# Kernel optimization log

Hardware: AMD Instinct MI355X
Metric: run time of the kernel (lower is better)

Reference implementation:

```python
import jax, jax.numpy as jnp
from jax import lax
import numpy as np

STATE_DIM, LATENT_DIM, HIDDEN_DIM = 18, 3, 16
BN_EPS = 1e-5


def _xavier(key, out_dim, in_dim):
    a = (6.0 / (in_dim + out_dim)) ** 0.5
    return jax.random.uniform(key, (out_dim, in_dim), minval=-a, maxval=a, dtype=jnp.float32)


def setup_inputs() -> dict:
    key = jax.random.key(0)
    ks = jax.random.split(key, 12)
    B, S, T = 4096, 256, 64
    inp = {
        "x_sequence": jax.random.normal(ks[0], (B, S, STATE_DIM), dtype=jnp.float32),
        "t_span": jnp.linspace(0.0, 6.3, T, dtype=jnp.float32),
        # encoder: Linear(18->16), ReLU, (Dropout off), BatchNorm1d(16, eval), Linear(16->3)
        "enc_w1": _xavier(ks[1], HIDDEN_DIM, STATE_DIM), "enc_b1": jnp.zeros((HIDDEN_DIM,), jnp.float32),
        "enc_bn_g": jnp.ones((HIDDEN_DIM,), jnp.float32), "enc_bn_b": jnp.zeros((HIDDEN_DIM,), jnp.float32),
        "enc_bn_m": jnp.zeros((HIDDEN_DIM,), jnp.float32), "enc_bn_v": jnp.ones((HIDDEN_DIM,), jnp.float32),
        "enc_w2": _xavier(ks[2], LATENT_DIM, HIDDEN_DIM), "enc_b2": jnp.zeros((LATENT_DIM,), jnp.float32),
        # decoder: Linear(3->16), ReLU, BN(16, eval), Linear(16->18)
        "dec_w1": _xavier(ks[3], HIDDEN_DIM, LATENT_DIM), "dec_b1": jnp.zeros((HIDDEN_DIM,), jnp.float32),
        "dec_bn_g": jnp.ones((HIDDEN_DIM,), jnp.float32), "dec_bn_b": jnp.zeros((HIDDEN_DIM,), jnp.float32),
        "dec_bn_m": jnp.zeros((HIDDEN_DIM,), jnp.float32), "dec_bn_v": jnp.ones((HIDDEN_DIM,), jnp.float32),
        "dec_w2": _xavier(ks[4], STATE_DIM, HIDDEN_DIM), "dec_b2": jnp.zeros((STATE_DIM,), jnp.float32),
        # ode_func: Linear(3->8), Tanh, Linear(8->3)
        "ode_w1": _xavier(ks[5], HIDDEN_DIM // 2, LATENT_DIM), "ode_b1": jnp.zeros((HIDDEN_DIM // 2,), jnp.float32),
        "ode_w2": _xavier(ks[6], LATENT_DIM, HIDDEN_DIM // 2), "ode_b2": jnp.zeros((LATENT_DIM,), jnp.float32),
        # perturbation classifier: Linear(3->4), ReLU, Linear(4->1), Sigmoid
        "cls_w1": _xavier(ks[7], 4, LATENT_DIM), "cls_b1": jnp.zeros((4,), jnp.float32),
        "cls_w2": _xavier(ks[8], 1, 4), "cls_b2": jnp.zeros((1,), jnp.float32),
    }
    return inp


def _bn_eval(x, g, b, m, v):
    return (x - m) * (g / jnp.sqrt(v + BN_EPS)) + b


def reference(x_sequence, t_span,
              enc_w1, enc_b1, enc_bn_g, enc_bn_b, enc_bn_m, enc_bn_v, enc_w2, enc_b2,
              dec_w1, dec_b1, dec_bn_g, dec_bn_b, dec_bn_m, dec_bn_v, dec_w2, dec_b2,
              ode_w1, ode_b1, ode_w2, ode_b2,
              cls_w1, cls_b1, cls_w2, cls_b2):
    B, S, D = x_sequence.shape
    T = t_span.shape[0]

    def encode(x):  # [N, 18] -> [N, 3]
        h = jax.nn.relu(x @ enc_w1.T + enc_b1)
        h = _bn_eval(h, enc_bn_g, enc_bn_b, enc_bn_m, enc_bn_v)
        return h @ enc_w2.T + enc_b2

    def decode(z):  # [N, 3] -> [N, 18]
        h = jax.nn.relu(z @ dec_w1.T + dec_b1)
        h = _bn_eval(h, dec_bn_g, dec_bn_b, dec_bn_m, dec_bn_v)
        return h @ dec_w2.T + dec_b2

    def ode_func(z):  # [B, 3] -> [B, 3]
        return jnp.tanh(z @ ode_w1.T + ode_b1) @ ode_w2.T + ode_b2

    x_flat = x_sequence.reshape(-1, D)              # [B*S, 18]
    z_flat = encode(x_flat)                         # [B*S, 3]
    z_seq = z_flat.reshape(B, S, LATENT_DIM)
    z0 = z_seq[:, -1, :]                            # [B, 3]

    # explicit Euler integration: z <- z + 0.1 * f(z), T steps
    def step(z, _):
        z_next = z + 0.1 * ode_func(z)
        return z_next, z_next

    _, z_traj = lax.scan(step, z0, None, length=T)  # [T, B, 3]
    z_pred = jnp.transpose(z_traj, (1, 0, 2))       # [B, T, 3]

    x_recon = decode(z_flat).reshape(B, S, D)
    x_pred = decode(z_pred.reshape(-1, LATENT_DIM)).reshape(B, T, D)

    z_mean = jnp.mean(z_seq, axis=1)                # [B, 3]
    h = jax.nn.relu(z_mean @ cls_w1.T + cls_b1)
    perturbation_prob = jax.nn.sigmoid(h @ cls_w2.T + cls_b2)  # [B, 1]

    return (x_recon, x_pred, perturbation_prob, z_seq)
```

## Files before the change

kernel.cpp:

```cpp
#include <hip/hip_runtime.h>
#include <math.h>

constexpr int Bn = 4096, Sn = 256, Tn = 64;
constexpr int Dn = 18, Hn = 16, Ln = 3;
constexpr float EPS = 1e-5f;

constexpr size_t OFF_XP   = (size_t)Bn * Sn * Dn;
constexpr size_t OFF_PROB = OFF_XP + (size_t)Bn * Tn * Dn;
constexpr size_t OFF_ZS   = OFF_PROB + (size_t)Bn;

__device__ __forceinline__ float fast_tanh(float x) {
    float ax = fabsf(x);
    float e  = __expf(-2.0f * ax);
    float r  = (1.0f - e) / (1.0f + e);
    return copysignf(r, x);
}

__global__ __launch_bounds__(256) void k1_encdec(
    const float* __restrict__ x,
    const float* __restrict__ ew1, const float* __restrict__ eb1,
    const float* __restrict__ eg,  const float* __restrict__ ebb,
    const float* __restrict__ em,  const float* __restrict__ ev,
    const float* __restrict__ ew2, const float* __restrict__ eb2,
    const float* __restrict__ dw1, const float* __restrict__ db1,
    const float* __restrict__ dg,  const float* __restrict__ dbn,
    const float* __restrict__ dm,  const float* __restrict__ dv,
    const float* __restrict__ dw2, const float* __restrict__ db2,
    const float* __restrict__ cw1, const float* __restrict__ cb1,
    const float* __restrict__ cw2, const float* __restrict__ cb2,
    float* __restrict__ xrec, float* __restrict__ prob, float* __restrict__ zseq)
{
    const int b = blockIdx.x;
    const int s = threadIdx.x;
    constexpr int TILE_F  = Sn * Dn;
    constexpr int TILE_F4 = TILE_F / 4;

    __shared__ float xt[TILE_F];
    __shared__ float esc[Hn], esh[Hn], dsc[Hn], dsh[Hn];
    __shared__ float red[4][3];

    if (s < Hn) {
        float sc = eg[s] / sqrtf(ev[s] + EPS);
        esc[s] = sc; esh[s] = ebb[s] - em[s] * sc;
        float sd = dg[s] / sqrtf(dv[s] + EPS);
        dsc[s] = sd; dsh[s] = dbn[s] - dm[s] * sd;
    }

    const float4* xg  = reinterpret_cast<const float4*>(x + (size_t)b * TILE_F);
    float4*       xt4 = reinterpret_cast<float4*>(xt);
    #pragma unroll
    for (int i = s; i < TILE_F4; i += 256) xt4[i] = xg[i];
    __syncthreads();

    float xv[Dn];
    #pragma unroll
    for (int k = 0; k < Dn; ++k) xv[k] = xt[s * Dn + k];

    float h[Hn];
    #pragma unroll
    for (int j = 0; j < Hn; ++j) {
        float a = eb1[j];
        #pragma unroll
        for (int k = 0; k < Dn; ++k) a = fmaf(ew1[j*Dn + k], xv[k], a);
        a = fmaxf(a, 0.0f);
        h[j] = fmaf(a, esc[j], esh[j]);
    }
    float z0 = eb2[0], z1 = eb2[1], z2 = eb2[2];
    #pragma unroll
    for (int j = 0; j < Hn; ++j) {
        z0 = fmaf(ew2[0*Hn + j], h[j], z0);
        z1 = fmaf(ew2[1*Hn + j], h[j], z1);
        z2 = fmaf(ew2[2*Hn + j], h[j], z2);
    }
    float* zp = zseq + ((size_t)b * Sn + s) * Ln;
    zp[0] = z0; zp[1] = z1; zp[2] = z2;

    float h2[Hn];
    #pragma unroll
    for (int j = 0; j < Hn; ++j) {
        float a = fmaf(dw1[j*Ln + 0], z0, db1[j]);
        a = fmaf(dw1[j*Ln + 1], z1, a);
        a = fmaf(dw1[j*Ln + 2], z2, a);
        a = fmaxf(a, 0.0f);
        h2[j] = fmaf(a, dsc[j], dsh[j]);
    }
    #pragma unroll
    for (int m = 0; m < Dn; ++m) {
        float a = db2[m];
        #pragma unroll
        for (int j = 0; j < Hn; ++j) a = fmaf(dw2[m*Hn + j], h2[j], a);
        xt[s * Dn + m] = a;
    }
    __syncthreads();

    float4* og = reinterpret_cast<float4*>(xrec + (size_t)b * TILE_F);
    #pragma unroll
    for (int i = s; i < TILE_F4; i += 256) og[i] = xt4[i];

    float r0 = z0, r1 = z1, r2 = z2;
    #pragma unroll
    for (int off = 32; off > 0; off >>= 1) {
        r0 += __shfl_down(r0, off);
        r1 += __shfl_down(r1, off);
        r2 += __shfl_down(r2, off);
    }
    const int lane = s & 63, wid = s >> 6;
    if (lane == 0) { red[wid][0] = r0; red[wid][1] = r1; red[wid][2] = r2; }
    __syncthreads();
    if (s == 0) {
        float m0 = (red[0][0] + red[1][0] + red[2][0] + red[3][0]) * (1.0f / Sn);
        float m1 = (red[0][1] + red[1][1] + red[2][1] + red[3][1]) * (1.0f / Sn);
        float m2 = (red[0][2] + red[1][2] + red[2][2] + red[3][2]) * (1.0f / Sn);
        float logit = cb2[0];
        #pragma unroll
        for (int j = 0; j < 4; ++j) {
            float a = fmaf(cw1[j*3 + 0], m0, cb1[j]);
            a = fmaf(cw1[j*3 + 1], m1, a);
            a = fmaf(cw1[j*3 + 2], m2, a);
            a = fmaxf(a, 0.0f);
            logit = fmaf(cw2[j], a, logit);
        }
        prob[b] = 1.0f / (1.0f + __expf(-logit));
    }
}

__global__ __launch_bounds__(256) void k2_ode(
    const float* __restrict__ zseq,
    const float* __restrict__ ow1, const float* __restrict__ ob1,
    const float* __restrict__ ow2, const float* __restrict__ ob2,
    float* __restrict__ zscr, int zlayout)
{
    const int b = blockIdx.x * blockDim.x + threadIdx.x;
    const float* zp = zseq + ((size_t)b * Sn + (Sn - 1)) * Ln;
    float z0 = zp[0], z1 = zp[1], z2 = zp[2];

    float w1[8][3], bb1[8], w2v[3][8], bb2[3];
    #pragma unroll
    for (int j = 0; j < 8; ++j) {
        bb1[j] = ob1[j];
        #pragma unroll
        for (int k = 0; k < 3; ++k) w1[j][k] = ow1[j*3 + k];
    }
    #pragma unroll
    for (int i = 0; i < 3; ++i) {
        bb2[i] = ob2[i];
        #pragma unroll
        for (int j = 0; j < 8; ++j) w2v[i][j] = ow2[i*8 + j];
    }

    for (int t = 0; t < Tn; ++t) {
        float a[8];
        #pragma unroll
        for (int j = 0; j < 8; ++j) {
            float u = fmaf(w1[j][0], z0, bb1[j]);
            u = fmaf(w1[j][1], z1, u);
            u = fmaf(w1[j][2], z2, u);
            a[j] = fast_tanh(u);
        }
        float d0 = bb2[0], d1 = bb2[1], d2 = bb2[2];
        #pragma unroll
        for (int j = 0; j < 8; ++j) {
            d0 = fmaf(w2v[0][j], a[j], d0);
            d1 = fmaf(w2v[1][j], a[j], d1);
            d2 = fmaf(w2v[2][j], a[j], d2);
        }
        z0 = fmaf(0.1f, d0, z0);
        z1 = fmaf(0.1f, d1, z1);
        z2 = fmaf(0.1f, d2, z2);
        size_t idx = (zlayout == 0) ? ((size_t)t * Bn + b) * Ln
                                    : ((size_t)b * Tn + t) * Dn;
        zscr[idx + 0] = z0; zscr[idx + 1] = z1; zscr[idx + 2] = z2;
    }
}

__global__ __launch_bounds__(256) void k3_decpred(
    const float* __restrict__ dw1, const float* __restrict__ db1,
    const float* __restrict__ dg,  const float* __restrict__ dbn,
    const float* __restrict__ dm,  const float* __restrict__ dv,
    const float* __restrict__ dw2, const float* __restrict__ db2,
    const float* __restrict__ zscr, int zlayout,
    float* __restrict__ xpred)
{
    const int r = blockIdx.x * blockDim.x + threadIdx.x;
    const int s = threadIdx.x;
    constexpr int TILE_F  = 256 * Dn;
    constexpr int TILE_F4 = TILE_F / 4;

    __shared__ float ot[TILE_F];
    __shared__ float dsc[Hn], dsh[Hn];
    if (s < Hn) {
        float sd = dg[s] / sqrtf(dv[s] + EPS);
        dsc[s] = sd;
        dsh[s] = dbn[s] - dm[s] * sd;
    }
    __syncthreads();

    const int bb = r / Tn, tt = r % Tn;
    size_t zidx = (zlayout == 0) ? ((size_t)tt * Bn + bb) * Ln
                                 : (size_t)r * Dn;
    float z0 = zscr[zidx + 0], z1 = zscr[zidx + 1], z2 = zscr[zidx + 2];

    float h2[Hn];
    #pragma unroll
    for (int j = 0; j < Hn; ++j) {
        float a = fmaf(dw1[j*Ln + 0], z0, db1[j]);
        a = fmaf(dw1[j*Ln + 1], z1, a);
        a = fmaf(dw1[j*Ln + 2], z2, a);
        a = fmaxf(a, 0.0f);
        h2[j] = fmaf(a, dsc[j], dsh[j]);
    }
    #pragma unroll
    for (int m = 0; m < Dn; ++m) {
        float a = db2[m];
        #pragma unroll
        for (int j = 0; j < Hn; ++j) a = fmaf(dw2[m*Hn + j], h2[j], a);
        ot[s * Dn + m] = a;
    }
    __syncthreads();

    float4* og = reinterpret_cast<float4*>(xpred + (size_t)blockIdx.x * TILE_F);
    const float4* ot4 = reinterpret_cast<const float4*>(ot);
    #pragma unroll
    for (int i = s; i < TILE_F4; i += 256) og[i] = ot4[i];
}

extern "C" void kernel_launch(void* const* d_in, const int* in_sizes, int n_in,
                              void* d_out, int out_size, void* d_ws, size_t ws_size,
                              hipStream_t stream)
{
    const float* x   = (const float*)d_in[0];
    const float* ew1 = (const float*)d_in[2];
    const float* eb1 = (const float*)d_in[3];
    const float* eg  = (const float*)d_in[4];
    const float* ebb = (const float*)d_in[5];
    const float* em  = (const float*)d_in[6];
    const float* ev  = (const float*)d_in[7];
    const float* ew2 = (const float*)d_in[8];
    const float* eb2 = (const float*)d_in[9];
    const float* dw1 = (const float*)d_in[10];
    const float* db1 = (const float*)d_in[11];
    const float* dg  = (const float*)d_in[12];
    const float* dbn = (const float*)d_in[13];
    const float* dm  = (const float*)d_in[14];
    const float* dv  = (const float*)d_in[15];
    const float* dw2 = (const float*)d_in[16];
    const float* db2 = (const float*)d_in[17];
    const float* ow1 = (const float*)d_in[18];
    const float* ob1 = (const float*)d_in[19];
    const float* ow2 = (const float*)d_in[20];
    const float* ob2 = (const float*)d_in[21];
    const float* cw1 = (const float*)d_in[22];
    const float* cb1 = (const float*)d_in[23];
    const float* cw2 = (const float*)d_in[24];
    const float* cb2 = (const float*)d_in[25];

    float* out   = (float*)d_out;
    float* xrec  = out;
    float* xpred = out + OFF_XP;
    float* prob  = out + OFF_PROB;
    float* zseq  = out + OFF_ZS;

    const size_t zbytes = (size_t)Bn * Tn * Ln * sizeof(float);
    float* zscr; int zlayout;
    if (ws_size >= zbytes) { zscr = (float*)d_ws; zlayout = 0; }
    else                   { zscr = xpred;        zlayout = 1; }

    k1_encdec<<<dim3(Bn), dim3(Sn), 0, stream>>>(
        x, ew1, eb1, eg, ebb, em, ev, ew2, eb2,
        dw1, db1, dg, dbn, dm, dv, dw2, db2,
        cw1, cb1, cw2, cb2, xrec, prob, zseq);

    k2_ode<<<dim3(Bn / 256), dim3(256), 0, stream>>>(
        zseq, ow1, ob1, ow2, ob2, zscr, zlayout);

    k3_decpred<<<dim3((Bn * Tn) / 256), dim3(256), 0, stream>>>(
        dw1, db1, dg, dbn, dm, dv, dw2, db2, zscr, zlayout, xpred);
}
```

Measured before the change: 262.4 us.

## Process multiple rows per thread and drop shared-memory staging in enc/dec kernels

```diff
diff --git a/kernel.cpp b/kernel.cpp
--- a/kernel.cpp
+++ b/kernel.cpp
@@ -4,6 +4,7 @@
 constexpr int Bn = 4096, Sn = 256, Tn = 64;
 constexpr int Dn = 18, Hn = 16, Ln = 3;
 constexpr float EPS = 1e-5f;
+constexpr int R = 4;
 
 constexpr size_t OFF_XP   = (size_t)Bn * Sn * Dn;
 constexpr size_t OFF_PROB = OFF_XP + (size_t)Bn * Tn * Dn;
@@ -30,101 +31,140 @@
     const float* __restrict__ cw2, const float* __restrict__ cb2,
     float* __restrict__ xrec, float* __restrict__ prob, float* __restrict__ zseq)
 {
-    const int b = blockIdx.x;
     const int s = threadIdx.x;
-    constexpr int TILE_F  = Sn * Dn;
-    constexpr int TILE_F4 = TILE_F / 4;
-
-    __shared__ float xt[TILE_F];
-    __shared__ float esc[Hn], esh[Hn], dsc[Hn], dsh[Hn];
-    __shared__ float red[4][3];
-
-    if (s < Hn) {
-        float sc = eg[s] / sqrtf(ev[s] + EPS);
-        esc[s] = sc; esh[s] = ebb[s] - em[s] * sc;
-        float sd = dg[s] / sqrtf(dv[s] + EPS);
-        dsc[s] = sd; dsh[s] = dbn[s] - dm[s] * sd;
-    }
-
-    const float4* xg  = reinterpret_cast<const float4*>(x + (size_t)b * TILE_F);
-    float4*       xt4 = reinterpret_cast<float4*>(xt);
-    #pragma unroll
-    for (int i = s; i < TILE_F4; i += 256) xt4[i] = xg[i];
+    const size_t row0 = (size_t)blockIdx.x * (R * Sn) + s;
+
+    float h[R][Hn];
+    #pragma unroll
+    for (int j = 0; j < Hn; ++j) {
+        float b = eb1[j];
+        #pragma unroll
+        for (int r = 0; r < R; ++r) h[r][j] = b;
+    }
+    #pragma unroll
+    for (int kk = 0; kk < Dn / 2; ++kk) {
+        float2 xa[R];
+        #pragma unroll
+        for (int r = 0; r < R; ++r)
+            xa[r] = *reinterpret_cast<const float2*>(x + (row0 + (size_t)r * Sn) * Dn + 2 * kk);
+        #pragma unroll
+        for (int j = 0; j < Hn; ++j) {
+            float w0 = ew1[j * Dn + 2 * kk];
+            float w1 = ew1[j * Dn + 2 * kk + 1];
+            #pragma unroll
+            for (int r = 0; r < R; ++r) {
+                h[r][j] = fmaf(w0, xa[r].x, h[r][j]);
+                h[r][j] = fmaf(w1, xa[r].y, h[r][j]);
+            }
+        }
+    }
+    #pragma unroll
+    for (int j = 0; j < Hn; ++j) {
+        float sc = eg[j] / sqrtf(ev[j] + EPS);
+        float sh = ebb[j] - em[j] * sc;
+        #pragma unroll
+        for (int r = 0; r < R; ++r)
+            h[r][j] = fmaf(fmaxf(h[r][j], 0.0f), sc, sh);
+    }
+
+    float zz[R][Ln];
+    #pragma unroll
+    for (int c = 0; c < Ln; ++c) {
+        float b = eb2[c];
+        #pragma unroll
+        for (int r = 0; r < R; ++r) zz[r][c] = b;
+    }
+    #pragma unroll
+    for (int j = 0; j < Hn; ++j) {
+        #pragma unroll
+        for (int c = 0; c < Ln; ++c) {
+            float w = ew2[c * Hn + j];
+            #pragma unroll
+            for (int r = 0; r < R; ++r) zz[r][c] = fmaf(w, h[r][j], zz[r][c]);
+        }
+    }
+    #pragma unroll
+    for (int r = 0; r < R; ++r) {
+        float* zp = zseq + (row0 + (size_t)r * Sn) * Ln;
+        zp[0] = zz[r][0]; zp[1] = zz[r][1]; zp[2] = zz[r][2];
+    }
+
+    float h2[R][Hn];
+    #pragma unroll
+    for (int j = 0; j < Hn; ++j) {
+        float w0 = dw1[j * Ln + 0], w1 = dw1[j * Ln + 1], w2 = dw1[j * Ln + 2];
+        float b  = db1[j];
+        float sc = dg[j] / sqrtf(dv[j] + EPS);
+        float sh = dbn[j] - dm[j] * sc;
+        #pragma unroll
+        for (int r = 0; r < R; ++r) {
+            float a = fmaf(w0, zz[r][0], b);
+            a = fmaf(w1, zz[r][1], a);
+            a = fmaf(w2, zz[r][2], a);
+            h2[r][j] = fmaf(fmaxf(a, 0.0f), sc, sh);
+        }
+    }
+    #pragma unroll
+    for (int m = 0; m < Dn; m += 2) {
+        float o0[R], o1[R];
+        #pragma unroll
+        for (int r = 0; r < R; ++r) { o0[r] = db2[m]; o1[r] = db2[m + 1]; }
+        #pragma unroll
+        for (int j = 0; j < Hn; ++j) {
+            float wa = dw2[m * Hn + j];
+            float wb = dw2[(m + 1) * Hn + j];
+            #pragma unroll
+            for (int r = 0; r < R; ++r) {
+                o0[r] = fmaf(wa, h2[r][j], o0[r]);
+                o1[r] = fmaf(wb, h2[r][j], o1[r]);
+            }
+        }
+        #pragma unroll
+        for (int r = 0; r < R; ++r)
+            *reinterpret_cast<float2*>(xrec + (row0 + (size_t)r * Sn) * Dn + m) =
+                make_float2(o0[r], o1[r]);
+    }
+
+    float acc[R][Ln];
+    #pragma unroll
+    for (int r = 0; r < R; ++r)
+        #pragma unroll
+        for (int c = 0; c < Ln; ++c) acc[r][c] = zz[r][c];
+    #pragma unroll
+    for (int off = 32; off > 0; off >>= 1) {
+        #pragma unroll
+        for (int r = 0; r < R; ++r)
+            #pragma unroll
+            for (int c = 0; c < Ln; ++c)
+                acc[r][c] += __shfl_down(acc[r][c], off);
+    }
+    __shared__ float red[4][R][Ln];
+    const int lane = s & 63, wid = s >> 6;
+    if (lane == 0) {
+        #pragma unroll
+        for (int r = 0; r < R; ++r)
+            #pragma unroll
+            for (int c = 0; c < Ln; ++c) red[wid][r][c] = acc[r][c];
+    }
     __syncthreads();
-
-    float xv[Dn];
-    #pragma unroll
-    for (int k = 0; k < Dn; ++k) xv[k] = xt[s * Dn + k];
-
-    float h[Hn];
-    #pragma unroll
-    for (int j = 0; j < Hn; ++j) {
-        float a = eb1[j];
-        #pragma unroll
-        for (int k = 0; k < Dn; ++k) a = fmaf(ew1[j*Dn + k], xv[k], a);
-        a = fmaxf(a, 0.0f);
-        h[j] = fmaf(a, esc[j], esh[j]);
-    }
-    float z0 = eb2[0], z1 = eb2[1], z2 = eb2[2];
-    #pragma unroll
-    for (int j = 0; j < Hn; ++j) {
-        z0 = fmaf(ew2[0*Hn + j], h[j], z0);
-        z1 = fmaf(ew2[1*Hn + j], h[j], z1);
-        z2 = fmaf(ew2[2*Hn + j], h[j], z2);
-    }
-    float* zp = zseq + ((size_t)b * Sn + s) * Ln;
-    zp[0] = z0; zp[1] = z1; zp[2] = z2;
-
-    float h2[Hn];
-    #pragma unroll
-    for (int j = 0; j < Hn; ++j) {
-        float a = fmaf(dw1[j*Ln + 0], z0, db1[j]);
-        a = fmaf(dw1[j*Ln + 1], z1, a);
-        a = fmaf(dw1[j*Ln + 2], z2, a);
-        a = fmaxf(a, 0.0f);
-        h2[j] = fmaf(a, dsc[j], dsh[j]);
-    }
-    #pragma unroll
-    for (int m = 0; m < Dn; ++m) {
-        float a = db2[m];
-        #pragma unroll
-        for (int j = 0; j < Hn; ++j) a = fmaf(dw2[m*Hn + j], h2[j], a);
-        xt[s * Dn + m] = a;
-    }
-    __syncthreads();
-
-    float4* og = reinterpret_cast<float4*>(xrec + (size_t)b * TILE_F);
-    #pragma unroll
-    for (int i = s; i < TILE_F4; i += 256) og[i] = xt4[i];
-
-    float r0 = z0, r1 = z1, r2 = z2;
-    #pragma unroll
-    for (int off = 32; off > 0; off >>= 1) {
-        r0 += __shfl_down(r0, off);
-        r1 += __shfl_down(r1, off);
-        r2 += __shfl_down(r2, off);
-    }
-    const int lane = s & 63, wid = s >> 6;
-    if (lane == 0) { red[wid][0] = r0; red[wid][1] = r1; red[wid][2] = r2; }
-    __syncthreads();
-    if (s == 0) {
-        float m0 = (red[0][0] + red[1][0] + red[2][0] + red[3][0]) * (1.0f / Sn);
-        float m1 = (red[0][1] + red[1][1] + red[2][1] + red[3][1]) * (1.0f / Sn);
-        float m2 = (red[0][2] + red[1][2] + red[2][2] + red[3][2]) * (1.0f / Sn);
+    if (s < R) {
+        float m0 = (red[0][s][0] + red[1][s][0] + red[2][s][0] + red[3][s][0]) * (1.0f / Sn);
+        float m1 = (red[0][s][1] + red[1][s][1] + red[2][s][1] + red[3][s][1]) * (1.0f / Sn);
+        float m2 = (red[0][s][2] + red[1][s][2] + red[2][s][2] + red[3][s][2]) * (1.0f / Sn);
         float logit = cb2[0];
         #pragma unroll
         for (int j = 0; j < 4; ++j) {
-            float a = fmaf(cw1[j*3 + 0], m0, cb1[j]);
-            a = fmaf(cw1[j*3 + 1], m1, a);
-            a = fmaf(cw1[j*3 + 2], m2, a);
+            float a = fmaf(cw1[j * 3 + 0], m0, cb1[j]);
+            a = fmaf(cw1[j * 3 + 1], m1, a);
+            a = fmaf(cw1[j * 3 + 2], m2, a);
             a = fmaxf(a, 0.0f);
             logit = fmaf(cw2[j], a, logit);
         }
-        prob[b] = 1.0f / (1.0f + __expf(-logit));
-    }
-}
-
-__global__ __launch_bounds__(256) void k2_ode(
+        prob[blockIdx.x * R + s] = 1.0f / (1.0f + __expf(-logit));
+    }
+}
+
+__global__ __launch_bounds__(64) void k2_ode(
     const float* __restrict__ zseq,
     const float* __restrict__ ow1, const float* __restrict__ ob1,
     const float* __restrict__ ow2, const float* __restrict__ ob2,
@@ -139,13 +179,13 @@
     for (int j = 0; j < 8; ++j) {
         bb1[j] = ob1[j];
         #pragma unroll
-        for (int k = 0; k < 3; ++k) w1[j][k] = ow1[j*3 + k];
+        for (int k = 0; k < 3; ++k) w1[j][k] = ow1[j * 3 + k];
     }
     #pragma unroll
     for (int i = 0; i < 3; ++i) {
         bb2[i] = ob2[i];
         #pragma unroll
-        for (int j = 0; j < 8; ++j) w2v[i][j] = ow2[i*8 + j];
+        for (int j = 0; j < 8; ++j) w2v[i][j] = ow2[i * 8 + j];
     }
 
     for (int t = 0; t < Tn; ++t) {
@@ -181,47 +221,55 @@
     const float* __restrict__ zscr, int zlayout,
     float* __restrict__ xpred)
 {
-    const int r = blockIdx.x * blockDim.x + threadIdx.x;
     const int s = threadIdx.x;
-    constexpr int TILE_F  = 256 * Dn;
-    constexpr int TILE_F4 = TILE_F / 4;
-
-    __shared__ float ot[TILE_F];
-    __shared__ float dsc[Hn], dsh[Hn];
-    if (s < Hn) {
-        float sd = dg[s] / sqrtf(dv[s] + EPS);
-        dsc[s] = sd;
-        dsh[s] = dbn[s] - dm[s] * sd;
-    }
-    __syncthreads();
-
-    const int bb = r / Tn, tt = r % Tn;
-    size_t zidx = (zlayout == 0) ? ((size_t)tt * Bn + bb) * Ln
-                                 : (size_t)r * Dn;
-    float z0 = zscr[zidx + 0], z1 = zscr[zidx + 1], z2 = zscr[zidx + 2];
-
-    float h2[Hn];
-    #pragma unroll
-    for (int j = 0; j < Hn; ++j) {
-        float a = fmaf(dw1[j*Ln + 0], z0, db1[j]);
-        a = fmaf(dw1[j*Ln + 1], z1, a);
-        a = fmaf(dw1[j*Ln + 2], z2, a);
-        a = fmaxf(a, 0.0f);
-        h2[j] = fmaf(a, dsc[j], dsh[j]);
-    }
-    #pragma unroll
-    for (int m = 0; m < Dn; ++m) {
-        float a = db2[m];
-        #pragma unroll
-        for (int j = 0; j < Hn; ++j) a = fmaf(dw2[m*Hn + j], h2[j], a);
-        ot[s * Dn + m] = a;
-    }
-    __syncthreads();
-
-    float4* og = reinterpret_cast<float4*>(xpred + (size_t)blockIdx.x * TILE_F);
-    const float4* ot4 = reinterpret_cast<const float4*>(ot);
-    #pragma unroll
-    for (int i = s; i < TILE_F4; i += 256) og[i] = ot4[i];
+    const size_t row0 = (size_t)blockIdx.x * (R * 256) + s;
+
+    float zz[R][Ln];
+    #pragma unroll
+    for (int r = 0; r < R; ++r) {
+        size_t row = row0 + (size_t)r * 256;
+        size_t zidx = (zlayout == 0) ? (((row & 63) * Bn + (row >> 6)) * Ln)
+                                     : row * Dn;
+        zz[r][0] = zscr[zidx + 0];
+        zz[r][1] = zscr[zidx + 1];
+        zz[r][2] = zscr[zidx + 2];
+    }
+
+    float h2[R][Hn];
+    #pragma unroll
+    for (int j = 0; j < Hn; ++j) {
+        float w0 = dw1[j * Ln + 0], w1 = dw1[j * Ln + 1], w2 = dw1[j * Ln + 2];
+        float b  = db1[j];
+        float sc = dg[j] / sqrtf(dv[j] + EPS);
+        float sh = dbn[j] - dm[j] * sc;
+        #pragma unroll
+        for (int r = 0; r < R; ++r) {
+            float a = fmaf(w0, zz[r][0], b);
+            a = fmaf(w1, zz[r][1], a);
+            a = fmaf(w2, zz[r][2], a);
+            h2[r][j] = fmaf(fmaxf(a, 0.0f), sc, sh);
+        }
+    }
+    #pragma unroll
+    for (int m = 0; m < Dn; m += 2) {
+        float o0[R], o1[R];
+        #pragma unroll
+        for (int r = 0; r < R; ++r) { o0[r] = db2[m]; o1[r] = db2[m + 1]; }
+        #pragma unroll
+        for (int j = 0; j < Hn; ++j) {
+            float wa = dw2[m * Hn + j];
+            float wb = dw2[(m + 1) * Hn + j];
+            #pragma unroll
+            for (int r = 0; r < R; ++r) {
+                o0[r] = fmaf(wa, h2[r][j], o0[r]);
+                o1[r] = fmaf(wb, h2[r][j], o1[r]);
+            }
+        }
+        #pragma unroll
+        for (int r = 0; r < R; ++r)
+            *reinterpret_cast<float2*>(xpred + (row0 + (size_t)r * 256) * Dn + m) =
+                make_float2(o0[r], o1[r]);
+    }
 }
 
 extern "C" void kernel_launch(void* const* d_in, const int* in_sizes, int n_in,
@@ -265,14 +313,14 @@
     if (ws_size >= zbytes) { zscr = (float*)d_ws; zlayout = 0; }
     else                   { zscr = xpred;        zlayout = 1; }
 
-    k1_encdec<<<dim3(Bn), dim3(Sn), 0, stream>>>(
+    k1_encdec<<<dim3(Bn / R), dim3(Sn), 0, stream>>>(
         x, ew1, eb1, eg, ebb, em, ev, ew2, eb2,
         dw1, db1, dg, dbn, dm, dv, dw2, db2,
         cw1, cb1, cw2, cb2, xrec, prob, zseq);
 
-    k2_ode<<<dim3(Bn / 256), dim3(256), 0, stream>>>(
+    k2_ode<<<dim3(Bn / 64), dim3(64), 0, stream>>>(
         zseq, ow1, ob1, ow2, ob2, zscr, zlayout);
 
-    k3_decpred<<<dim3((Bn * Tn) / 256), dim3(256), 0, stream>>>(
+    k3_decpred<<<dim3((Bn * Tn) / (R * 256)), dim3(256), 0, stream>>>(
         dw1, db1, dg, dbn, dm, dv, dw2, db2, zscr, zlayout, xpred);
 }
```

Result: slower. 293.3 us (+11.7%).
